# Kernel optimization log

Hardware: AMD Instinct MI355X
Metric: run time of the kernel (lower is better)

## Reference

```python
import jax, jax.numpy as jnp
import numpy as np

HIDDEN = 768
PDIM = int(HIDDEN / 4.67)  # 164
QK_DIM = 16
EPS = 1e-5


def setup_inputs() -> dict:
    key = jax.random.key(0)
    k_hs, k_qkv, k_out = jax.random.split(key, 3)
    B, S = 8, 2048
    hidden_states = jax.random.normal(k_hs, (B, S, HIDDEN), dtype=jnp.float32)
    qkv_out = 2 * QK_DIM + PDIM  # 196
    qkv_w = jax.random.normal(k_qkv, (qkv_out, PDIM), dtype=jnp.float32) * (PDIM ** -0.5)
    qkv_b = jnp.zeros((qkv_out,), dtype=jnp.float32)
    out_w = jax.random.normal(k_out, (HIDDEN, HIDDEN), dtype=jnp.float32) * (HIDDEN ** -0.5)
    out_b = jnp.zeros((HIDDEN,), dtype=jnp.float32)
    ln_scale = jnp.ones((PDIM,), dtype=jnp.float32)
    ln_bias = jnp.zeros((PDIM,), dtype=jnp.float32)
    return {
        "hidden_states": hidden_states,
        "ln_scale": ln_scale,
        "ln_bias": ln_bias,
        "qkv_w": qkv_w,
        "qkv_b": qkv_b,
        "out_w": out_w,
        "out_b": out_b,
    }


def reference(hidden_states, ln_scale, ln_bias, qkv_w, qkv_b, out_w, out_b):
    # channel split
    x1 = hidden_states[..., :PDIM]   # [B,S,pdim]
    x2 = hidden_states[..., PDIM:]   # [B,S,hidden-pdim]
    # LayerNorm over last dim
    mean = jnp.mean(x1, axis=-1, keepdims=True)
    var = jnp.mean(jnp.square(x1 - mean), axis=-1, keepdims=True)
    x1n = (x1 - mean) * jax.lax.rsqrt(var + EPS) * ln_scale + ln_bias
    # qkv projection: [B,S,2*qk+pdim]
    qkv = jnp.einsum("bsd,od->bso", x1n, qkv_w) + qkv_b
    q = qkv[..., :QK_DIM]
    k = qkv[..., QK_DIM:2 * QK_DIM]
    v = qkv[..., 2 * QK_DIM:]
    scale = QK_DIM ** -0.5
    scores = jnp.einsum("bqd,bkd->bqk", q, k) * scale  # [B,S,S]
    probs = jax.nn.softmax(scores, axis=-1)
    attended = jnp.einsum("bqk,bkd->bqd", probs, v)  # [B,S,pdim]
    merged = jnp.concatenate([attended, x2], axis=-1)  # [B,S,hidden]
    out = jnp.einsum("bsd,od->bso", merged, out_w) + out_b
    return out
```

## Files before the change

kernel.cpp:

```cpp
#include <hip/hip_runtime.h>
#include <hip/hip_bf16.h>

#define HID 768
#define PD 164
#define NQ 196
#define SEQ 2048

typedef __attribute__((ext_vector_type(8))) short bf16x8_t;
typedef __attribute__((ext_vector_type(4))) float f32x4_t;
typedef __attribute__((ext_vector_type(16))) float f32x16_t;
typedef __attribute__((ext_vector_type(4))) unsigned int u32x4_t;

static __device__ __forceinline__ unsigned short f2bfu(float f) {
  union { __hip_bfloat16 h; unsigned short u; } cv;
  cv.h = __float2bfloat16(f);
  return cv.u;
}

static __device__ __forceinline__ unsigned cvtpk(float a, float b) {
  unsigned r;
  asm("v_cvt_pk_bf16_f32 %0, %1, %2" : "=v"(r) : "v"(a), "v"(b));
  return r;
}

static __device__ __forceinline__ void gload16(const void* g, void* l) {
  __builtin_amdgcn_global_load_lds(
      (const __attribute__((address_space(1))) void*)g,
      (__attribute__((address_space(3))) void*)l, 16, 0, 0);
}

__global__ __launch_bounds__(256) void k_prep(const float* __restrict__ qkv_w,
                                              const float* __restrict__ out_w,
                                              unsigned short* __restrict__ qwb,
                                              unsigned short* __restrict__ wb) {
  int bid = blockIdx.x;
  if (bid < 576) {
    int i = (bid * 256 + threadIdx.x) * 4;
    float4 v = *(const float4*)(out_w + i);
    ushort4 o;
    o.x = f2bfu(v.x); o.y = f2bfu(v.y); o.z = f2bfu(v.z); o.w = f2bfu(v.w);
    *(ushort4*)(wb + i) = o;
  } else {
    int i = ((bid - 576) * 256 + threadIdx.x) * 4;
    int n = i / 192, k = i - n * 192;
    float v0 = (n < NQ && k + 0 < PD) ? qkv_w[n * PD + k + 0] : 0.f;
    float v1 = (n < NQ && k + 1 < PD) ? qkv_w[n * PD + k + 1] : 0.f;
    float v2 = (n < NQ && k + 2 < PD) ? qkv_w[n * PD + k + 2] : 0.f;
    float v3 = (n < NQ && k + 3 < PD) ? qkv_w[n * PD + k + 3] : 0.f;
    ushort4 o;
    o.x = f2bfu(v0); o.y = f2bfu(v1); o.z = f2bfu(v2); o.w = f2bfu(v3);
    *(ushort4*)(qwb + i) = o;
  }
}

__global__ __launch_bounds__(256) void k_ln(const float* __restrict__ hidden,
                                            const float* __restrict__ lns,
                                            const float* __restrict__ lnb,
                                            unsigned short* __restrict__ x1n,
                                            unsigned short* __restrict__ merged) {
  __shared__ float xr[64][172];
  __shared__ float stats[64][2];
  int t = threadIdx.x;
  int r0 = blockIdx.x * 64;
  #pragma unroll
  for (int i = 0; i < 11; i++) {
    int idx = t + i * 256;
    if (idx < 2624) {
      int row = idx / 41, q = idx - row * 41;
      float4 v = *(const float4*)(hidden + (size_t)(r0 + row) * HID + q * 4);
      *(float4*)&xr[row][q * 4] = v;
    }
  }
  __syncthreads();
  {
    int l = t & 63, w = t >> 6;
    int row = w * 16 + (l & 15), g = l >> 4;
    float sum = 0.f, sq = 0.f;
    #pragma unroll
    for (int j = 0; j < 41; j++) {
      float x = xr[row][g * 41 + j];
      sum += x; sq += x * x;
    }
    sum += __shfl_xor(sum, 16, 64); sum += __shfl_xor(sum, 32, 64);
    sq  += __shfl_xor(sq, 16, 64);  sq  += __shfl_xor(sq, 32, 64);
    float mean = sum * (1.f / PD);
    float var = sq * (1.f / PD) - mean * mean;
    float rstd = rsqrtf(var + 1e-5f);
    if (g == 0) { stats[row][0] = mean; stats[row][1] = rstd; }
  }
  __syncthreads();
  #pragma unroll
  for (int i = 0; i < 24; i++) {
    int idx = t + i * 256;
    int row = idx / 96, c2 = idx - row * 96;
    int d = c2 * 2;
    float mean = stats[row][0], rstd = stats[row][1];
    float v0 = (d < PD)     ? (xr[row][d]     - mean) * rstd * lns[d]     + lnb[d]     : 0.f;
    float v1 = (d + 1 < PD) ? (xr[row][d + 1] - mean) * rstd * lns[d + 1] + lnb[d + 1] : 0.f;
    unsigned int pk = (unsigned int)f2bfu(v0) | ((unsigned int)f2bfu(v1) << 16);
    *(unsigned int*)(x1n + (size_t)(r0 + row) * 192 + d) = pk;
  }
  #pragma unroll
  for (int i = 0; i < 38; i++) {
    int idx = t + i * 256;
    if (idx < 9664) {
      int row = idx / 151, q = idx - row * 151;
      int d = PD + q * 4;
      float4 v = *(const float4*)(hidden + (size_t)(r0 + row) * HID + d);
      ushort4 o;
      o.x = f2bfu(v.x); o.y = f2bfu(v.y); o.z = f2bfu(v.z); o.w = f2bfu(v.w);
      *(ushort4*)(merged + (size_t)(r0 + row) * HID + d) = o;
    }
  }
}

__global__ __launch_bounds__(256) void k_qkv(const unsigned short* __restrict__ x1n,
                                             const unsigned short* __restrict__ qwb,
                                             const float* __restrict__ qkv_b,
                                             unsigned short* __restrict__ qg,
                                             unsigned short* __restrict__ kg,
                                             unsigned short* __restrict__ v16) {
  __shared__ unsigned short Al[64 * 64];
  __shared__ unsigned short Bl[208 * 64];
  int t = threadIdx.x;
  int m0 = blockIdx.x * 64;
  int l = t & 63, w = t >> 6;
  f32x4_t acc[13];
  #pragma unroll
  for (int n = 0; n < 13; n++) acc[n] = (f32x4_t){0.f, 0.f, 0.f, 0.f};
  for (int ks = 0; ks < 3; ks++) {
    #pragma unroll
    for (int i = 0; i < 2; i++) {
      int off = t + i * 256;
      int row = off >> 3, c = off & 7;
      gload16(x1n + (size_t)(m0 + row) * 192 + ks * 64 + c * 8, (char*)Al + off * 16);
    }
    #pragma unroll
    for (int i = 0; i < 7; i++) {
      int off = t + i * 256;
      if (off < 1664) {
        int row = off >> 3, c = off & 7;
        gload16(qwb + (size_t)row * 192 + ks * 64 + c * 8, (char*)Bl + off * 16);
      }
    }
    __syncthreads();
    #pragma unroll
    for (int kc = 0; kc < 2; kc++) {
      bf16x8_t a = *(const bf16x8_t*)(Al + (w * 16 + (l & 15)) * 64 + kc * 32 + (l >> 4) * 8);
      #pragma unroll
      for (int n = 0; n < 13; n++) {
        bf16x8_t b = *(const bf16x8_t*)(Bl + (n * 16 + (l & 15)) * 64 + kc * 32 + (l >> 4) * 8);
        acc[n] = __builtin_amdgcn_mfma_f32_16x16x32_bf16(a, b, acc[n], 0, 0, 0);
      }
    }
    __syncthreads();
  }
  int g = l >> 4;
  #pragma unroll
  for (int n = 0; n < 13; n++) {
    int col = n * 16 + (l & 15);
    float bias = (col < NQ) ? qkv_b[col] : 0.f;
    #pragma unroll
    for (int r = 0; r < 4; r++) {
      int grow = m0 + w * 16 + g * 4 + r;
      float v = acc[n][r] + bias;
      if (col < 16) {
        qg[(size_t)grow * 16 + col] = f2bfu(v * 0.36067376022224085f);
      } else if (col < 32) {
        kg[(size_t)grow * 16 + (col - 16)] = f2bfu(v);
      } else {
        int d = col - 32;
        float ov = (d == 164) ? 1.0f : ((d < PD) ? v : 0.0f);
        int bb = grow >> 11, s = grow & 2047;
        v16[(((size_t)(bb * 128 + (s >> 4))) * 192 + d) * 16 + (s & 15)] = f2bfu(ov);
      }
    }
  }
}

__global__ __launch_bounds__(256) void k_attn(const unsigned short* __restrict__ qg,
                                              const unsigned short* __restrict__ kg,
                                              const unsigned short* __restrict__ v16,
                                              unsigned short* __restrict__ merged) {
  __shared__ float red[2][64 * 98];
  int t = threadIdx.x;
  int w = t >> 6, l = t & 63;
  int b = blockIdx.x & 7, qt = blockIdx.x >> 3;
  int lo = l & 31, hi = l >> 5;
  int qbase = b * SEQ + qt * 32;
  bf16x8_t qf = *(const bf16x8_t*)(qg + (size_t)(qbase + lo) * 16 + hi * 8);
  const unsigned short* kb = kg + (size_t)b * SEQ * 16;
  const unsigned short* vbb = v16 + (size_t)b * 128 * 192 * 16;
  f32x16_t zro;
  #pragma unroll
  for (int r = 0; r < 16; r++) zro[r] = 0.f;
  f32x16_t acc[6];
  #pragma unroll
  for (int f = 0; f < 6; f++) acc[f] = zro;

  int it0 = w * 8;
  for (int it = it0; it < it0 + 8; ++it) {
    bf16x8_t kf0 = *(const bf16x8_t*)(kb + (size_t)(it * 64 + lo) * 16 + hi * 8);
    bf16x8_t kf1 = *(const bf16x8_t*)(kb + (size_t)(it * 64 + 32 + lo) * 16 + hi * 8);
    bf16x8_t va[6], vb_[6];
    {
      const unsigned short* vt0 = vbb + (size_t)(it * 4) * (192 * 16) + hi * 8;
      #pragma unroll
      for (int f = 0; f < 6; f++) va[f] = *(const bf16x8_t*)(vt0 + (f * 32 + lo) * 16);
    }
    f32x16_t sc0 = __builtin_amdgcn_mfma_f32_32x32x16_bf16(kf0, qf, zro, 0, 0, 0);
    f32x16_t sc1 = __builtin_amdgcn_mfma_f32_32x32x16_bf16(kf1, qf, zro, 0, 0, 0);
    bf16x8_t pa[4];
    #pragma unroll
    for (int jt = 0; jt < 2; ++jt) {
      f32x16_t sc = jt ? sc1 : sc0;
      unsigned u[8], x[8];
      #pragma unroll
      for (int k = 0; k < 8; ++k)
        u[k] = cvtpk(exp2f(sc[2 * k]), exp2f(sc[2 * k + 1]));
      #pragma unroll
      for (int k = 0; k < 8; ++k)
        x[k] = (unsigned)__shfl_xor((int)u[k], 32, 64);
      u32x4_t w0, w1;
      if (hi == 0) {
        w0 = (u32x4_t){u[0], u[1], x[0], x[1]};
        w1 = (u32x4_t){u[4], u[5], x[4], x[5]};
      } else {
        w0 = (u32x4_t){x[2], x[3], u[2], u[3]};
        w1 = (u32x4_t){x[6], x[7], u[6], u[7]};
      }
      union { u32x4_t u4; bf16x8_t h8; } c0, c1;
      c0.u4 = w0; c1.u4 = w1;
      pa[jt * 2 + 0] = c0.h8;
      pa[jt * 2 + 1] = c1.h8;
    }
#define PV_STEP(JS, VCUR, VNXT, PREF)                                              \
    {                                                                              \
      if (PREF) {                                                                  \
        const unsigned short* vtn = vbb + (size_t)(it * 4 + (JS) + 1) * (192 * 16) + hi * 8; \
        _Pragma("unroll")                                                          \
        for (int f = 0; f < 6; f++) VNXT[f] = *(const bf16x8_t*)(vtn + (f * 32 + lo) * 16); \
      }                                                                            \
      _Pragma("unroll")                                                            \
      for (int f = 0; f < 6; f++)                                                  \
        acc[f] = __builtin_amdgcn_mfma_f32_32x32x16_bf16(pa[JS], VCUR[f], acc[f], 0, 0, 0); \
    }
    PV_STEP(0, va,  vb_, 1)
    PV_STEP(1, vb_, va,  1)
    PV_STEP(2, va,  vb_, 1)
    PV_STEP(3, vb_, va,  0)
#undef PV_STEP
  }

  if (w >= 2) {
    float* dst = &red[w - 2][l * 98];
    #pragma unroll
    for (int f = 0; f < 6; f++)
      #pragma unroll
      for (int r = 0; r < 16; r += 2)
        *(float2*)(dst + f * 16 + r) = make_float2(acc[f][r], acc[f][r + 1]);
  }
  __syncthreads();
  if (w < 2) {
    const float* src = &red[w][l * 98];
    #pragma unroll
    for (int f = 0; f < 6; f++)
      #pragma unroll
      for (int r = 0; r < 16; r += 2) {
        float2 v = *(const float2*)(src + f * 16 + r);
        acc[f][r] += v.x; acc[f][r + 1] += v.y;
      }
  }
  __syncthreads();
  if (w == 1) {
    float* dst = &red[0][l * 98];
    #pragma unroll
    for (int f = 0; f < 6; f++)
      #pragma unroll
      for (int r = 0; r < 16; r += 2)
        *(float2*)(dst + f * 16 + r) = make_float2(acc[f][r], acc[f][r + 1]);
  }
  __syncthreads();
  if (w == 0) {
    const float* src = &red[0][l * 98];
    #pragma unroll
    for (int f = 0; f < 6; f++)
      #pragma unroll
      for (int r = 0; r < 16; r += 2) {
        float2 v = *(const float2*)(src + f * 16 + r);
        acc[f][r] += v.x; acc[f][r + 1] += v.y;
      }
    float dninv[16];
    #pragma unroll
    for (int r = 0; r < 16; ++r)
      dninv[r] = 1.0f / __shfl(acc[5][r], 4 + hi * 32, 64);
    #pragma unroll
    for (int f = 0; f < 6; ++f) {
      int d = f * 32 + lo;
      if (d < PD) {
        #pragma unroll
        for (int r = 0; r < 16; ++r) {
          int q = qbase + (r & 3) + 8 * (r >> 2) + 4 * hi;
          merged[(size_t)q * HID + d] = f2bfu(acc[f][r] * dninv[r]);
        }
      }
    }
  }
}

__global__ __launch_bounds__(256) void k_out(const unsigned short* __restrict__ mg,
                                             const unsigned short* __restrict__ wb,
                                             const float* __restrict__ out_b,
                                             float* __restrict__ out) {
  __shared__ unsigned short Al[2][128 * 64];
  __shared__ unsigned short Bl[2][128 * 64];
  int t = threadIdx.x;
  int bid = blockIdx.x;
  int wgid = (bid & 7) * 96 + (bid >> 3);
  int nb = wgid % 6, mb = wgid / 6;
  int m0 = mb * 128, n0 = nb * 128;
  int l = t & 63, w = t >> 6, wr = w >> 1, wc = w & 1;
  int lr = l & 15, lg = l >> 4;
  f32x4_t acc[4][4];
  #pragma unroll
  for (int mi = 0; mi < 4; mi++)
    #pragma unroll
    for (int ni = 0; ni < 4; ni++) acc[mi][ni] = (f32x4_t){0.f, 0.f, 0.f, 0.f};

  auto stage = [&](int buf, int kt) {
    #pragma unroll
    for (int i = 0; i < 4; i++) {
      int off = t + i * 256;
      int row = off >> 3, c = off & 7;
      gload16(mg + (size_t)(m0 + row) * HID + kt * 64 + c * 8, (char*)&Al[buf][0] + off * 16);
    }
    #pragma unroll
    for (int i = 0; i < 4; i++) {
      int off = t + i * 256;
      int row = off >> 3, c = off & 7;
      gload16(wb + (size_t)(n0 + row) * HID + kt * 64 + c * 8, (char*)&Bl[buf][0] + off * 16);
    }
  };
  auto compute = [&](int cur) {
    __builtin_amdgcn_s_setprio(1);
    #pragma unroll
    for (int kc = 0; kc < 2; kc++) {
      bf16x8_t a[4], bfr[4];
      #pragma unroll
      for (int mi = 0; mi < 4; mi++)
        a[mi] = *(const bf16x8_t*)(&Al[cur][(wr * 64 + mi * 16 + lr) * 64 + kc * 32 + lg * 8]);
      #pragma unroll
      for (int ni = 0; ni < 4; ni++)
        bfr[ni] = *(const bf16x8_t*)(&Bl[cur][(wc * 64 + ni * 16 + lr) * 64 + kc * 32 + lg * 8]);
      #pragma unroll
      for (int mi = 0; mi < 4; mi++)
        #pragma unroll
        for (int ni = 0; ni < 4; ni++)
          acc[mi][ni] = __builtin_amdgcn_mfma_f32_16x16x32_bf16(a[mi], bfr[ni], acc[mi][ni], 0, 0, 0);
    }
    __builtin_amdgcn_s_setprio(0);
  };

  stage(0, 0);
  stage(1, 1);
  for (int kt = 0; kt < 11; kt++) {
    int cur = kt & 1;
    asm volatile("s_waitcnt vmcnt(8)" ::: "memory");
    __builtin_amdgcn_sched_barrier(0);
    __builtin_amdgcn_s_barrier();
    compute(cur);
    asm volatile("s_waitcnt lgkmcnt(0)" ::: "memory");
    __builtin_amdgcn_sched_barrier(0);
    __builtin_amdgcn_s_barrier();
    if (kt + 2 < 12) stage(cur, kt + 2);
  }
  asm volatile("s_waitcnt vmcnt(0)" ::: "memory");
  __builtin_amdgcn_sched_barrier(0);
  __builtin_amdgcn_s_barrier();
  compute(1);

  #pragma unroll
  for (int ni = 0; ni < 4; ni++) {
    int col = n0 + wc * 64 + ni * 16 + lr;
    float bias = out_b[col];
    #pragma unroll
    for (int mi = 0; mi < 4; mi++) {
      #pragma unroll
      for (int r = 0; r < 4; r++) {
        int row = m0 + wr * 64 + mi * 16 + lg * 4 + r;
        out[(size_t)row * HID + col] = acc[mi][ni][r] + bias;
      }
    }
  }
}

extern "C" void kernel_launch(void* const* d_in, const int* in_sizes, int n_in,
                              void* d_out, int out_size, void* d_ws, size_t ws_size,
                              hipStream_t stream) {
  const float* hidden = (const float*)d_in[0];
  const float* lns    = (const float*)d_in[1];
  const float* lnb    = (const float*)d_in[2];
  const float* qkv_w  = (const float*)d_in[3];
  const float* qkv_b  = (const float*)d_in[4];
  const float* out_w  = (const float*)d_in[5];
  const float* out_b  = (const float*)d_in[6];
  char* ws = (char*)d_ws;
  unsigned short* qg  = (unsigned short*)(ws + 0);
  unsigned short* kg  = (unsigned short*)(ws + 524288);
  unsigned short* v16 = (unsigned short*)(ws + 1048576);
  unsigned short* x1n = (unsigned short*)(ws + 7340032);
  unsigned short* qwb = (unsigned short*)(ws + 13631488);
  unsigned short* wb  = (unsigned short*)(ws + 13711360);
  unsigned short* mg  = (unsigned short*)(ws + 14891008);
  hipLaunchKernelGGL(k_prep, dim3(615), dim3(256), 0, stream, qkv_w, out_w, qwb, wb);
  hipLaunchKernelGGL(k_ln,   dim3(256), dim3(256), 0, stream, hidden, lns, lnb, x1n, mg);
  hipLaunchKernelGGL(k_qkv,  dim3(256), dim3(256), 0, stream, x1n, qwb, qkv_b, qg, kg, v16);
  hipLaunchKernelGGL(k_attn, dim3(512), dim3(256), 0, stream, qg, kg, v16, mg);
  hipLaunchKernelGGL(k_out,  dim3(768), dim3(256), 0, stream, mg, wb, out_b, (float*)d_out);
}
```

Baseline: 103.3 us.

## Vectorize V stores, permlane swap in attention, prefetch K/V, swizzle out-proj LDS

The QKV epilogue is restructured so the q and k tiles are written directly and V is stored as packed ushort4 vectors instead of scalar scattered stores. The attention kernel replaces shuffle-based P repacking with v_permlane32_swap, software-pipelines K and the first V tile loads across iterations, and sets a two-waves-per-SIMD launch bound. The output projection GEMM applies an XOR swizzle to its LDS tiles to avoid bank conflicts. The prefetch reads one tile past the end of each wave's range, which is extra work and may read past the batch's K/V data for the last wave.

Result: faster. 100.6 us (-2.7%).

```diff
diff --git a/kernel.cpp b/kernel.cpp
--- a/kernel.cpp
+++ b/kernel.cpp
@@ -155,33 +155,45 @@
     }
     __syncthreads();
   }
-  int g = l >> 4;
-  #pragma unroll
-  for (int n = 0; n < 13; n++) {
-    int col = n * 16 + (l & 15);
-    float bias = (col < NQ) ? qkv_b[col] : 0.f;
+  int g = l >> 4, lr15 = l & 15;
+  {
+    float bias = qkv_b[lr15];
     #pragma unroll
     for (int r = 0; r < 4; r++) {
       int grow = m0 + w * 16 + g * 4 + r;
-      float v = acc[n][r] + bias;
-      if (col < 16) {
-        qg[(size_t)grow * 16 + col] = f2bfu(v * 0.36067376022224085f);
-      } else if (col < 32) {
-        kg[(size_t)grow * 16 + (col - 16)] = f2bfu(v);
-      } else {
-        int d = col - 32;
-        float ov = (d == 164) ? 1.0f : ((d < PD) ? v : 0.0f);
-        int bb = grow >> 11, s = grow & 2047;
-        v16[(((size_t)(bb * 128 + (s >> 4))) * 192 + d) * 16 + (s & 15)] = f2bfu(ov);
-      }
-    }
-  }
-}
-
-__global__ __launch_bounds__(256) void k_attn(const unsigned short* __restrict__ qg,
-                                              const unsigned short* __restrict__ kg,
-                                              const unsigned short* __restrict__ v16,
-                                              unsigned short* __restrict__ merged) {
+      qg[(size_t)grow * 16 + lr15] = f2bfu((acc[0][r] + bias) * 0.36067376022224085f);
+    }
+  }
+  {
+    float bias = qkv_b[16 + lr15];
+    #pragma unroll
+    for (int r = 0; r < 4; r++) {
+      int grow = m0 + w * 16 + g * 4 + r;
+      kg[(size_t)grow * 16 + lr15] = f2bfu(acc[1][r] + bias);
+    }
+  }
+  int s0 = (m0 & 2047) + w * 16;
+  int bb = m0 >> 11;
+  size_t vrowbase = (size_t)(bb * 128 + (s0 >> 4)) * 192;
+  #pragma unroll
+  for (int n = 2; n < 13; n++) {
+    int col = n * 16 + lr15;
+    int d = col - 32;
+    float bias = (col < NQ) ? qkv_b[col] : 0.f;
+    float v0 = acc[n][0] + bias, v1 = acc[n][1] + bias;
+    float v2 = acc[n][2] + bias, v3 = acc[n][3] + bias;
+    if (d == 164) { v0 = v1 = v2 = v3 = 1.f; }
+    else if (d >= PD) { v0 = v1 = v2 = v3 = 0.f; }
+    ushort4 o;
+    o.x = f2bfu(v0); o.y = f2bfu(v1); o.z = f2bfu(v2); o.w = f2bfu(v3);
+    *(ushort4*)(v16 + (vrowbase + d) * 16 + g * 4) = o;
+  }
+}
+
+__global__ __launch_bounds__(256, 2) void k_attn(const unsigned short* __restrict__ qg,
+                                                 const unsigned short* __restrict__ kg,
+                                                 const unsigned short* __restrict__ v16,
+                                                 unsigned short* __restrict__ merged) {
   __shared__ float red[2][64 * 98];
   int t = threadIdx.x;
   int w = t >> 6, l = t & 63;
@@ -199,57 +211,52 @@
   for (int f = 0; f < 6; f++) acc[f] = zro;
 
   int it0 = w * 8;
+  bf16x8_t kf0 = *(const bf16x8_t*)(kb + (size_t)(it0 * 64 + lo) * 16 + hi * 8);
+  bf16x8_t kf1 = *(const bf16x8_t*)(kb + (size_t)(it0 * 64 + 32 + lo) * 16 + hi * 8);
+  bf16x8_t va[6], vb_[6];
+  {
+    const unsigned short* vt0 = vbb + (size_t)(it0 * 4) * (192 * 16) + hi * 8;
+    #pragma unroll
+    for (int f = 0; f < 6; f++) va[f] = *(const bf16x8_t*)(vt0 + (f * 32 + lo) * 16);
+  }
   for (int it = it0; it < it0 + 8; ++it) {
-    bf16x8_t kf0 = *(const bf16x8_t*)(kb + (size_t)(it * 64 + lo) * 16 + hi * 8);
-    bf16x8_t kf1 = *(const bf16x8_t*)(kb + (size_t)(it * 64 + 32 + lo) * 16 + hi * 8);
-    bf16x8_t va[6], vb_[6];
-    {
-      const unsigned short* vt0 = vbb + (size_t)(it * 4) * (192 * 16) + hi * 8;
-      #pragma unroll
-      for (int f = 0; f < 6; f++) va[f] = *(const bf16x8_t*)(vt0 + (f * 32 + lo) * 16);
-    }
+    bf16x8_t nk0 = *(const bf16x8_t*)(kb + (size_t)((it + 1) * 64 + lo) * 16 + hi * 8);
+    bf16x8_t nk1 = *(const bf16x8_t*)(kb + (size_t)((it + 1) * 64 + 32 + lo) * 16 + hi * 8);
     f32x16_t sc0 = __builtin_amdgcn_mfma_f32_32x32x16_bf16(kf0, qf, zro, 0, 0, 0);
     f32x16_t sc1 = __builtin_amdgcn_mfma_f32_32x32x16_bf16(kf1, qf, zro, 0, 0, 0);
     bf16x8_t pa[4];
     #pragma unroll
     for (int jt = 0; jt < 2; ++jt) {
       f32x16_t sc = jt ? sc1 : sc0;
-      unsigned u[8], x[8];
+      unsigned u[8];
       #pragma unroll
       for (int k = 0; k < 8; ++k)
         u[k] = cvtpk(exp2f(sc[2 * k]), exp2f(sc[2 * k + 1]));
-      #pragma unroll
-      for (int k = 0; k < 8; ++k)
-        x[k] = (unsigned)__shfl_xor((int)u[k], 32, 64);
-      u32x4_t w0, w1;
-      if (hi == 0) {
-        w0 = (u32x4_t){u[0], u[1], x[0], x[1]};
-        w1 = (u32x4_t){u[4], u[5], x[4], x[5]};
-      } else {
-        w0 = (u32x4_t){x[2], x[3], u[2], u[3]};
-        w1 = (u32x4_t){x[6], x[7], u[6], u[7]};
-      }
+      asm volatile("v_permlane32_swap_b32 %0, %1" : "+v"(u[0]), "+v"(u[2]));
+      asm volatile("v_permlane32_swap_b32 %0, %1" : "+v"(u[1]), "+v"(u[3]));
+      asm volatile("v_permlane32_swap_b32 %0, %1" : "+v"(u[4]), "+v"(u[6]));
+      asm volatile("v_permlane32_swap_b32 %0, %1" : "+v"(u[5]), "+v"(u[7]));
       union { u32x4_t u4; bf16x8_t h8; } c0, c1;
-      c0.u4 = w0; c1.u4 = w1;
+      c0.u4 = (u32x4_t){u[0], u[1], u[2], u[3]};
+      c1.u4 = (u32x4_t){u[4], u[5], u[6], u[7]};
       pa[jt * 2 + 0] = c0.h8;
       pa[jt * 2 + 1] = c1.h8;
     }
-#define PV_STEP(JS, VCUR, VNXT, PREF)                                              \
-    {                                                                              \
-      if (PREF) {                                                                  \
-        const unsigned short* vtn = vbb + (size_t)(it * 4 + (JS) + 1) * (192 * 16) + hi * 8; \
-        _Pragma("unroll")                                                          \
-        for (int f = 0; f < 6; f++) VNXT[f] = *(const bf16x8_t*)(vtn + (f * 32 + lo) * 16); \
-      }                                                                            \
-      _Pragma("unroll")                                                            \
-      for (int f = 0; f < 6; f++)                                                  \
+#define PV_STEP(JS, VCUR, VNXT, NT, NJS)                                            \
+    {                                                                               \
+      const unsigned short* vtn = vbb + (size_t)((NT) * 4 + (NJS)) * (192 * 16) + hi * 8; \
+      _Pragma("unroll")                                                             \
+      for (int f = 0; f < 6; f++) VNXT[f] = *(const bf16x8_t*)(vtn + (f * 32 + lo) * 16); \
+      _Pragma("unroll")                                                             \
+      for (int f = 0; f < 6; f++)                                                   \
         acc[f] = __builtin_amdgcn_mfma_f32_32x32x16_bf16(pa[JS], VCUR[f], acc[f], 0, 0, 0); \
     }
-    PV_STEP(0, va,  vb_, 1)
-    PV_STEP(1, vb_, va,  1)
-    PV_STEP(2, va,  vb_, 1)
-    PV_STEP(3, vb_, va,  0)
+    PV_STEP(0, va,  vb_, it, 1)
+    PV_STEP(1, vb_, va,  it, 2)
+    PV_STEP(2, va,  vb_, it, 3)
+    PV_STEP(3, vb_, va,  it + 1, 0)
 #undef PV_STEP
+    kf0 = nk0; kf1 = nk1;
   }
 
   if (w >= 2) {
@@ -332,13 +339,15 @@
     for (int i = 0; i < 4; i++) {
       int off = t + i * 256;
       int row = off >> 3, c = off & 7;
-      gload16(mg + (size_t)(m0 + row) * HID + kt * 64 + c * 8, (char*)&Al[buf][0] + off * 16);
+      int cs = c ^ (row & 7);
+      gload16(mg + (size_t)(m0 + row) * HID + kt * 64 + cs * 8, (char*)&Al[buf][0] + off * 16);
     }
     #pragma unroll
     for (int i = 0; i < 4; i++) {
       int off = t + i * 256;
       int row = off >> 3, c = off & 7;
-      gload16(wb + (size_t)(n0 + row) * HID + kt * 64 + c * 8, (char*)&Bl[buf][0] + off * 16);
+      int cs = c ^ (row & 7);
+      gload16(wb + (size_t)(n0 + row) * HID + kt * 64 + cs * 8, (char*)&Bl[buf][0] + off * 16);
     }
   };
   auto compute = [&](int cur) {
@@ -348,10 +357,10 @@
       bf16x8_t a[4], bfr[4];
       #pragma unroll
       for (int mi = 0; mi < 4; mi++)
-        a[mi] = *(const bf16x8_t*)(&Al[cur][(wr * 64 + mi * 16 + lr) * 64 + kc * 32 + lg * 8]);
+        a[mi] = *(const bf16x8_t*)(&Al[cur][(wr * 64 + mi * 16 + lr) * 64 + (((kc * 4 + lg) ^ (lr & 7)) * 8)]);
       #pragma unroll
       for (int ni = 0; ni < 4; ni++)
-        bfr[ni] = *(const bf16x8_t*)(&Bl[cur][(wc * 64 + ni * 16 + lr) * 64 + kc * 32 + lg * 8]);
+        bfr[ni] = *(const bf16x8_t*)(&Bl[cur][(wc * 64 + ni * 16 + lr) * 64 + (((kc * 4 + lg) ^ (lr & 7)) * 8)]);
       #pragma unroll
       for (int mi = 0; mi < 4; mi++)
         #pragma unroll
```
